# Kernel optimization log

Measured on AMD Instinct MI355X. Metric: run time of the kernel, lower is better.

## Reference

```python
import jax, jax.numpy as jnp
import numpy as np


def setup_inputs() -> dict:
    key = jax.random.key(0)
    k1, k2, k3 = jax.random.split(key, 3)
    T, B, H = 2048, 16, 512
    inputs = jax.random.normal(k1, (T, B, H), dtype=jnp.float32)
    # torch.rand override of the context vector, made explicit/deterministic
    rand_ctx = jax.random.uniform(k2, (T, B, H), dtype=jnp.float32)
    # xavier_uniform_ with relu gain: bound = gain * sqrt(6/(fan_in+fan_out))
    gain = float(np.sqrt(2.0))
    bound = gain * float(np.sqrt(6.0 / (H + H)))
    W = jax.random.uniform(k3, (H, H), dtype=jnp.float32, minval=-bound, maxval=bound)
    return {"inputs": inputs, "rand_ctx": rand_ctx, "W": W, "attention_width": 3}


def reference(inputs, rand_ctx, W, attention_width):
    # inputs: [T, B, H]; attention_width is dead code in the original (lb=0 always)
    T, B, H = inputs.shape
    # Context half of the output: inputs[t] for t<2, random override for t>=2
    t_col = jnp.arange(T)[:, None, None]
    ctx = jnp.where(t_col < 2, inputs, rand_ctx)               # [T, B, H]
    results = jnp.concatenate([inputs, ctx], axis=-1)          # [T, B, 2H]

    # Attention weights (detached in the original, never fed to the output):
    # scores[b, t, s] = (x_t W) . x_s, softmax over s < t, only for t >= 2
    q = jnp.einsum('tbh,hk->tbk', inputs, W)                   # [T, B, H]
    scores = jnp.einsum('tbk,sbk->bts', q, inputs)             # [B, T, T]
    t_idx = jnp.arange(T)
    mask = (t_idx[None, :] < t_idx[:, None]) & (t_idx[:, None] >= 2)  # [T, T]
    neg = jnp.finfo(scores.dtype).min
    attn = jax.nn.softmax(jnp.where(mask[None], scores, neg), axis=-1)
    attn = jnp.where(mask[None], attn, jnp.zeros((), scores.dtype))   # zero padded rows
    return results, attn
```

## Files before the change

### kernel.cpp

```cpp
#include <hip/hip_runtime.h>
#include <math.h>

#define T_DIM 2048
#define B_DIM 16
#define H_DIM 512
#define NKB   (H_DIM / 32)

typedef _Float16 f16x8 __attribute__((ext_vector_type(8)));
typedef float f32x4 __attribute__((ext_vector_type(4)));

__device__ __forceinline__ unsigned short h_bits(_Float16 h) {
    unsigned short u; __builtin_memcpy(&u, &h, 2); return u;
}

__device__ __forceinline__ size_t tile_off(int rowblk, int kblk) {
    return ((size_t)rowblk * NKB + kblk) * 4096;
}
__device__ __forceinline__ size_t tiled_idx(int r, int c) {
    return tile_off(r >> 7, c >> 5) + (size_t)((c >> 3) & 3) * 1024 + (size_t)(r & 127) * 8 + (c & 7);
}

__global__ __launch_bounds__(256) void k_prep(const float* __restrict__ X,
                                              const float* __restrict__ RC,
                                              const float* __restrict__ W,
                                              float* __restrict__ out,
                                              unsigned short* __restrict__ Xh,
                                              unsigned short* __restrict__ Wth) {
    if (blockIdx.x >= 8192) {
        int i = (blockIdx.x - 8192) * 256 + threadIdx.x;
        int n = i & 511;
        int k0 = (i >> 9) * 8;
        unsigned int hw[4];
#pragma unroll
        for (int e = 0; e < 4; ++e) {
            _Float16 h0 = (_Float16)W[(size_t)(k0 + 2 * e) * H_DIM + n];
            _Float16 h1 = (_Float16)W[(size_t)(k0 + 2 * e + 1) * H_DIM + n];
            hw[e] = (unsigned int)h_bits(h0) | ((unsigned int)h_bits(h1) << 16);
        }
        *(uint4*)(Wth + tiled_idx(n, k0)) = make_uint4(hw[0], hw[1], hw[2], hw[3]);
        return;
    }
    int i = blockIdx.x * 256 + threadIdx.x;
    int row = i >> 6;
    int h0 = (i & 63) * 8;
    int t = row >> 4;
    int b = row & 15;
    const float* xp = X + (size_t)row * H_DIM + h0;
    float4 v0 = *(const float4*)xp;
    float4 v1 = *(const float4*)(xp + 4);
    float* op = out + (size_t)row * (2 * H_DIM) + h0;
    *(float4*)op = v0;
    *(float4*)(op + 4) = v1;
    const float* cp = RC + (size_t)row * H_DIM + h0;
    float4 c0 = *(const float4*)cp;
    float4 c1 = *(const float4*)(cp + 4);
    if (t < 2) { c0 = v0; c1 = v1; }
    *(float4*)(op + H_DIM) = c0;
    *(float4*)(op + H_DIM + 4) = c1;
    float xs[8] = {v0.x, v0.y, v0.z, v0.w, v1.x, v1.y, v1.z, v1.w};
    unsigned int hw[4];
#pragma unroll
    for (int e = 0; e < 4; ++e) {
        _Float16 a = (_Float16)xs[2 * e], bb = (_Float16)xs[2 * e + 1];
        hw[e] = (unsigned int)h_bits(a) | ((unsigned int)h_bits(bb) << 16);
    }
    int r = b * T_DIM + t;
    *(uint4*)(Xh + tiled_idx(r, h0)) = make_uint4(hw[0], hw[1], hw[2], hw[3]);
}

__device__ __forceinline__ void stage_half(const unsigned short* __restrict__ src_tile,
                                           unsigned short* lds_base, int lane, int h) {
#pragma unroll
    for (int c = 0; c < 4; ++c) {
        const int ch = h * 4 + c;
        __builtin_amdgcn_global_load_lds(
            (const __attribute__((address_space(1))) void*)(src_tile + ch * 512 + lane * 8),
            (__attribute__((address_space(3))) void*)(lds_base + ch * 512),
            16, 0, 0);
    }
}

__global__ __launch_bounds__(256) void k_qgemm_mfma(const unsigned short* __restrict__ Xh,
                                                    const unsigned short* __restrict__ Wth,
                                                    unsigned short* __restrict__ Qh) {
    __shared__ __align__(16) unsigned short Ah[2][4][128][8], Bh[2][4][128][8];
    const int bid = blockIdx.x;
    const int swz = (bid & 7) * 128 + (bid >> 3);
    const int mblk = swz >> 2, nblk = swz & 3;
    const int m0 = mblk * 128, n0 = nblk * 128;
    const int tid = threadIdx.x, lane = tid & 63, w = tid >> 6;
    const int t_off = (w >> 1) * 64, s_off = (w & 1) * 64;
    const int l15 = lane & 15, lg = lane >> 4;
    f32x4 acc[4][4] = {};

    for (int ksp = 0; ksp < NKB / 2; ++ksp) {
        if (ksp) __syncthreads();
        if (w < 2) {
            stage_half(Xh + tile_off(mblk, 2 * ksp),     &Ah[0][0][0][0], lane, w);
            stage_half(Xh + tile_off(mblk, 2 * ksp + 1), &Ah[1][0][0][0], lane, w);
        } else {
            stage_half(Wth + tile_off(nblk, 2 * ksp),     &Bh[0][0][0][0], lane, w - 2);
            stage_half(Wth + tile_off(nblk, 2 * ksp + 1), &Bh[1][0][0][0], lane, w - 2);
        }
        __syncthreads();

#pragma unroll
        for (int kk = 0; kk < 2; ++kk) {
            f16x8 ah[4], bh[4];
#pragma unroll
            for (int i2 = 0; i2 < 4; ++i2)
                ah[i2] = *(const f16x8*)&Ah[kk][lg][t_off + i2 * 16 + l15][0];
#pragma unroll
            for (int j = 0; j < 4; ++j)
                bh[j] = *(const f16x8*)&Bh[kk][lg][s_off + j * 16 + l15][0];
#pragma unroll
            for (int i2 = 0; i2 < 4; ++i2)
#pragma unroll
                for (int j = 0; j < 4; ++j)
                    acc[i2][j] = __builtin_amdgcn_mfma_f32_16x16x32_f16(ah[i2], bh[j], acc[i2][j], 0, 0, 0);
        }
    }

#pragma unroll
    for (int i2 = 0; i2 < 4; ++i2)
#pragma unroll
        for (int j = 0; j < 4; ++j)
#pragma unroll
            for (int r = 0; r < 4; ++r) {
                int R = m0 + t_off + i2 * 16 + lg * 4 + r;
                int C = n0 + s_off + j * 16 + l15;
                _Float16 qh = (_Float16)acc[i2][j][r];
                Qh[tiled_idx(R, C)] = h_bits(qh);
            }
}

__global__ __launch_bounds__(256) void k_scores_mfma(const unsigned short* __restrict__ Qh,
                                                     const unsigned short* __restrict__ Xh,
                                                     float* __restrict__ attn) {
    const int bid = blockIdx.x;
    const int swz = (bid & 7) * 272 + (bid >> 3);
    const int b = swz / 136;
    const int r = swz - b * 136;
    int ti = (int)((sqrtf(8.f * (float)r + 1.f) - 1.f) * 0.5f);
    while ((ti + 1) * (ti + 2) / 2 <= r) ++ti;
    while (ti * (ti + 1) / 2 > r) --ti;
    const int si = r - ti * (ti + 1) / 2;
    const int t0 = ti * 128, s0 = si * 128;

    __shared__ __align__(16) unsigned short Ah[2][4][128][8], Bh[2][4][128][8];
    const int tid = threadIdx.x, lane = tid & 63, w = tid >> 6;
    const int t_off = (w >> 1) * 64, s_off = (w & 1) * 64;
    const int l15 = lane & 15, lg = lane >> 4;
    const int ablk = b * (T_DIM / 128) + ti;
    const int bblk = b * (T_DIM / 128) + si;
    f32x4 acc[4][4] = {};

    for (int ksp = 0; ksp < NKB / 2; ++ksp) {
        if (ksp) __syncthreads();
        if (w < 2) {
            stage_half(Qh + tile_off(ablk, 2 * ksp),     &Ah[0][0][0][0], lane, w);
            stage_half(Qh + tile_off(ablk, 2 * ksp + 1), &Ah[1][0][0][0], lane, w);
        } else {
            stage_half(Xh + tile_off(bblk, 2 * ksp),     &Bh[0][0][0][0], lane, w - 2);
            stage_half(Xh + tile_off(bblk, 2 * ksp + 1), &Bh[1][0][0][0], lane, w - 2);
        }
        __syncthreads();

#pragma unroll
        for (int kk = 0; kk < 2; ++kk) {
            f16x8 ah[4], bh[4];
#pragma unroll
            for (int i2 = 0; i2 < 4; ++i2)
                ah[i2] = *(const f16x8*)&Ah[kk][lg][t_off + i2 * 16 + l15][0];
#pragma unroll
            for (int j = 0; j < 4; ++j)
                bh[j] = *(const f16x8*)&Bh[kk][lg][s_off + j * 16 + l15][0];
#pragma unroll
            for (int i2 = 0; i2 < 4; ++i2)
#pragma unroll
                for (int j = 0; j < 4; ++j)
                    acc[i2][j] = __builtin_amdgcn_mfma_f32_16x16x32_f16(ah[i2], bh[j], acc[i2][j], 0, 0, 0);
        }
    }

    float* base = attn + (size_t)b * T_DIM * T_DIM;
#pragma unroll
    for (int i2 = 0; i2 < 4; ++i2)
#pragma unroll
        for (int j = 0; j < 4; ++j)
#pragma unroll
            for (int rr = 0; rr < 4; ++rr) {
                int t = t0 + t_off + i2 * 16 + lg * 4 + rr;
                int s = s0 + s_off + j * 16 + l15;
                base[(size_t)t * T_DIM + s] = acc[i2][j][rr];
            }
}

__global__ __launch_bounds__(256) void k_softmax(float* __restrict__ attn) {
    const int row = blockIdx.x;
    const int t = row & (T_DIM - 1);
    float* p = attn + (size_t)row * T_DIM;
    const int tid = threadIdx.x;
    const int n = (t >= 2) ? t : 0;
    __shared__ float redm[4], redl[4];

    if (n == 0) {
        const float4 z = {0.f, 0.f, 0.f, 0.f};
        for (int s = tid * 4; s < T_DIM; s += 1024) *(float4*)&p[s] = z;
        return;
    }

    float m = -1e30f, l = 0.f;
    for (int s = tid * 4; s < n; s += 1024) {
        float v[4];
        int cnt;
        if (s + 3 < n) {
            float4 q = *(const float4*)&p[s];
            v[0] = q.x; v[1] = q.y; v[2] = q.z; v[3] = q.w; cnt = 4;
        } else {
            cnt = n - s;
            for (int j = 0; j < cnt; ++j) v[j] = p[s + j];
        }
        float vm = v[0];
        for (int j = 1; j < cnt; ++j) vm = fmaxf(vm, v[j]);
        if (vm > m) { l *= expf(m - vm); m = vm; }
        for (int j = 0; j < cnt; ++j) l += expf(v[j] - m);
    }
#pragma unroll
    for (int off = 32; off >= 1; off >>= 1) {
        float mo = __shfl_xor(m, off);
        float lo = __shfl_xor(l, off);
        float M = fmaxf(m, mo);
        l = l * expf(m - M) + lo * expf(mo - M);
        m = M;
    }
    if ((tid & 63) == 0) { redm[tid >> 6] = m; redl[tid >> 6] = l; }
    __syncthreads();
    {
        float M = fmaxf(fmaxf(redm[0], redm[1]), fmaxf(redm[2], redm[3]));
        float L = redl[0] * expf(redm[0] - M) + redl[1] * expf(redm[1] - M)
                + redl[2] * expf(redm[2] - M) + redl[3] * expf(redm[3] - M);
        m = M;
        l = L;
    }
    const float inv = 1.f / l;

    for (int s = tid * 4; s < T_DIM; s += 1024) {
        float4 o = {0.f, 0.f, 0.f, 0.f};
        if (s + 3 < n) {
            float4 v = *(float4*)&p[s];
            o.x = expf(v.x - m) * inv;
            o.y = expf(v.y - m) * inv;
            o.z = expf(v.z - m) * inv;
            o.w = expf(v.w - m) * inv;
        } else if (s < n) {
            float tmp[4] = {0.f, 0.f, 0.f, 0.f};
            for (int j = 0; j < 4; ++j)
                if (s + j < n) tmp[j] = expf(p[s + j] - m) * inv;
            o.x = tmp[0]; o.y = tmp[1]; o.z = tmp[2]; o.w = tmp[3];
        }
        *(float4*)&p[s] = o;
    }
}

extern "C" void kernel_launch(void* const* d_in, const int* in_sizes, int n_in,
                              void* d_out, int out_size, void* d_ws, size_t ws_size,
                              hipStream_t stream) {
    const float* inputs   = (const float*)d_in[0];
    const float* rand_ctx = (const float*)d_in[1];
    const float* W        = (const float*)d_in[2];
    float* out  = (float*)d_out;
    float* attn = out + (size_t)T_DIM * B_DIM * 2 * H_DIM;

    unsigned short* Xh  = (unsigned short*)d_ws;
    unsigned short* Qh  = Xh + (size_t)33554432;
    unsigned short* Wth = Xh + (size_t)67108864;

    k_prep<<<dim3(8192 + 128), dim3(256), 0, stream>>>(
        inputs, rand_ctx, W, out, Xh, Wth);

    k_qgemm_mfma<<<dim3(1024), dim3(256), 0, stream>>>(Xh, Wth, Qh);

    k_scores_mfma<<<dim3(2176), dim3(256), 0, stream>>>(Qh, Xh, attn);

    k_softmax<<<dim3(B_DIM * T_DIM), dim3(256), 0, stream>>>(attn);
}
```

Baseline: 308.5 us.

## Store attention scores as fp16 in place and single-pass register softmax

The score GEMM now writes its results as fp16 into the first half of each fp32 output row instead of writing full fp32 values. The softmax kernel has each thread load 8 fp16 values once into registers, computes max and sum from them, and writes the expanded fp32 probabilities over the whole row. This roughly halves the intermediate write and read traffic and removes the second read pass over each row. In exchange, scores are rounded to fp16 before the softmax, which adds rounding error to the output. The fp16 buffer is read in place, so correctness depends on every thread finishing its reads before the barrier, after which the row is overwritten.

```diff
diff --git a/kernel.cpp b/kernel.cpp
--- a/kernel.cpp
+++ b/kernel.cpp
@@ -11,6 +11,9 @@
 
 __device__ __forceinline__ unsigned short h_bits(_Float16 h) {
     unsigned short u; __builtin_memcpy(&u, &h, 2); return u;
+}
+__device__ __forceinline__ float h2f(unsigned short u) {
+    _Float16 h; __builtin_memcpy(&h, &u, 2); return (float)h;
 }
 
 __device__ __forceinline__ size_t tile_off(int rowblk, int kblk) {
@@ -192,7 +195,8 @@
             for (int rr = 0; rr < 4; ++rr) {
                 int t = t0 + t_off + i2 * 16 + lg * 4 + rr;
                 int s = s0 + s_off + j * 16 + l15;
-                base[(size_t)t * T_DIM + s] = acc[i2][j][rr];
+                _Float16 hv = (_Float16)acc[i2][j][rr];
+                ((unsigned short*)(base + (size_t)t * T_DIM))[s] = h_bits(hv);
             }
 }
 
@@ -206,28 +210,29 @@
 
     if (n == 0) {
         const float4 z = {0.f, 0.f, 0.f, 0.f};
-        for (int s = tid * 4; s < T_DIM; s += 1024) *(float4*)&p[s] = z;
+        *(float4*)&p[tid * 8] = z;
+        *(float4*)&p[tid * 8 + 4] = z;
         return;
     }
 
+    const int sbase = tid * 8;
+    uint4 rv = *(const uint4*)((const unsigned short*)p + sbase);
+    float v[8];
+    v[0] = h2f((unsigned short)(rv.x & 0xffff)); v[1] = h2f((unsigned short)(rv.x >> 16));
+    v[2] = h2f((unsigned short)(rv.y & 0xffff)); v[3] = h2f((unsigned short)(rv.y >> 16));
+    v[4] = h2f((unsigned short)(rv.z & 0xffff)); v[5] = h2f((unsigned short)(rv.z >> 16));
+    v[6] = h2f((unsigned short)(rv.w & 0xffff)); v[7] = h2f((unsigned short)(rv.w >> 16));
+
     float m = -1e30f, l = 0.f;
-    for (int s = tid * 4; s < n; s += 1024) {
-        float v[4];
-        int cnt;
-        if (s + 3 < n) {
-            float4 q = *(const float4*)&p[s];
-            v[0] = q.x; v[1] = q.y; v[2] = q.z; v[3] = q.w; cnt = 4;
-        } else {
-            cnt = n - s;
-            for (int j = 0; j < cnt; ++j) v[j] = p[s + j];
-        }
-        float vm = v[0];
-        for (int j = 1; j < cnt; ++j) vm = fmaxf(vm, v[j]);
-        if (vm > m) { l *= expf(m - vm); m = vm; }
-        for (int j = 0; j < cnt; ++j) l += expf(v[j] - m);
-    }
-#pragma unroll
-    for (int off = 32; off >= 1; off >>= 1) {
+#pragma unroll
+    for (int j = 0; j < 8; ++j)
+        if (sbase + j < n) m = fmaxf(m, v[j]);
+#pragma unroll
+    for (int j = 0; j < 8; ++j)
+        if (sbase + j < n) l += expf(v[j] - m);
+
+#pragma unroll
+    for (int off = 1; off <= 32; off <<= 1) {
         float mo = __shfl_xor(m, off);
         float lo = __shfl_xor(l, off);
         float M = fmaxf(m, mo);
@@ -245,22 +250,14 @@
     }
     const float inv = 1.f / l;
 
-    for (int s = tid * 4; s < T_DIM; s += 1024) {
-        float4 o = {0.f, 0.f, 0.f, 0.f};
-        if (s + 3 < n) {
-            float4 v = *(float4*)&p[s];
-            o.x = expf(v.x - m) * inv;
-            o.y = expf(v.y - m) * inv;
-            o.z = expf(v.z - m) * inv;
-            o.w = expf(v.w - m) * inv;
-        } else if (s < n) {
-            float tmp[4] = {0.f, 0.f, 0.f, 0.f};
-            for (int j = 0; j < 4; ++j)
-                if (s + j < n) tmp[j] = expf(p[s + j] - m) * inv;
-            o.x = tmp[0]; o.y = tmp[1]; o.z = tmp[2]; o.w = tmp[3];
-        }
-        *(float4*)&p[s] = o;
-    }
+    float o[8];
+#pragma unroll
+    for (int j = 0; j < 8; ++j)
+        o[j] = (sbase + j < n) ? expf(v[j] - m) * inv : 0.f;
+    float4 o0 = {o[0], o[1], o[2], o[3]};
+    float4 o1 = {o[4], o[5], o[6], o[7]};
+    *(float4*)&p[sbase] = o0;
+    *(float4*)&p[sbase + 4] = o1;
 }
 
 extern "C" void kernel_launch(void* const* d_in, const int* in_sizes, int n_in,
```

New measurement: 293.6 us (median of 2 runs). -4.8%, faster.
